# Optimization experiments

Measured on AMD Instinct MI355X. Metric: run time of the kernel, lower is better.

## Reference

```python
import jax, jax.numpy as jnp
import numpy as np

SIGNAL_LENGTH = 2048
BASE_STEP_SIZE = 0.01
MAX_ITERATIONS = 15
STEP_DECAY = 0.9
MIN_STEP = 1e-4
POS_TOL = 1e-4
EPS_SCALES = (0.001, 0.003, 0.01)
EPS_WEIGHTS = (0.5, 0.3, 0.2)


def setup_inputs() -> dict:
    key = jax.random.key(0)
    k1, k2 = jax.random.split(key)
    batch = 32768
    initial_predictions = jax.random.uniform(k1, (batch, 3), dtype=jnp.float32)
    signals = jax.random.normal(k2, (batch, SIGNAL_LENGTH), dtype=jnp.float32)
    return {"initial_predictions": initial_predictions, "signals": signals}


def _sample(signals, positions):
    # signals: [B, L], positions in [0,1]: [B, P] -> values [B, P]
    L = SIGNAL_LENGTH
    p = jnp.clip(positions * (L - 1), 0.0, float(L - 1))
    il = jnp.clip(jnp.floor(p).astype(jnp.int32), 0, L - 1)
    ir = jnp.clip(jnp.ceil(p).astype(jnp.int32), 0, L - 1)
    vl = jnp.take_along_axis(signals, il, axis=1)
    vr = jnp.take_along_axis(signals, ir, axis=1)
    wr = p - il.astype(p.dtype)
    return (1.0 - wr) * vl + wr * vr


def _grads_and_curvs(signals, positions):
    g_acc = 0.0
    c_acc = 0.0
    for eps, w in zip(EPS_SCALES, EPS_WEIGHTS):
        pc = jnp.clip(positions, eps, 1.0 - eps)
        v = _sample(signals, pc)
        vl = _sample(signals, pc - eps)
        vr = _sample(signals, pc + eps)
        g_acc = g_acc + w * (vr - vl) / (2.0 * eps)
        c_acc = c_acc + w * (vr + vl - 2.0 * v) / (eps * eps)
    return g_acc, jnp.clip(c_acc, -1000.0, 1000.0)


def _refine(initial_predictions, signals):
    positions = initial_predictions
    prev_positions = positions
    best_positions = positions
    best_values = _sample(signals, positions)
    step_size0 = jnp.asarray(BASE_STEP_SIZE, dtype=positions.dtype)
    done0 = jnp.asarray(False)

    def body(carry, it):
        positions, prev, best_pos, best_val, step_size, done = carry
        g, c = _grads_and_curvs(signals, positions)
        step = -g / (jnp.abs(c) + 1e-6)
        max_step = 0.2 * (STEP_DECAY ** it)
        step = jnp.clip(step, -max_step, max_step)
        new_pos = jnp.clip(positions + step_size * step, 0.0, 1.0)
        cur_val = _sample(signals, new_pos)
        # NOTE: original code sets best_positions = positions.clone() then
        # where(mask, positions, best_positions) -> best_positions == new_pos always
        new_best_pos = new_pos
        new_best_val = jnp.where(cur_val > best_val, cur_val, best_val)
        pos_change = jnp.max(jnp.abs(new_pos - prev))
        stop = (pos_change < POS_TOL) | (step_size < MIN_STEP)
        new_step = jnp.where(stop, step_size, step_size * STEP_DECAY)
        new_prev = jnp.where(stop, prev, new_pos)
        sel = lambda n, o: jnp.where(done, o, n)
        carry = (sel(new_pos, positions), sel(new_prev, prev),
                 sel(new_best_pos, best_pos), sel(new_best_val, best_val),
                 jnp.where(done, step_size, new_step), done | stop)
        return carry, None

    its = jnp.arange(MAX_ITERATIONS, dtype=positions.dtype)
    carry0 = (positions, prev_positions, best_positions, best_values, step_size0, done0)
    (_, _, best_positions, _, _, _), _ = jax.lax.scan(body, carry0, its)
    return best_positions


def reference(initial_predictions, signals):
    if signals.ndim == 3:
        signals = signals[:, 0, :]
    return _refine(initial_predictions, signals)
```

## Files before the change

kernel.cpp:

```cpp
#include <hip/hip_runtime.h>

#define SIG_LEN 2048
#define LM1F 2047.0f
#define N_ITER 15
#define TPB 128
#define WIN 96
#define WPAD 97

__device__ __forceinline__ float sample_lds(const float* __restrict__ w, float q) {
    float p = __fmul_rn(q, LM1F);
    p = fminf(fmaxf(p, 0.0f), LM1F);
    float fl = floorf(p);
    int il = (int)fl;
    int inc = (p > fl) ? 1 : 0;
    float wr = __fsub_rn(p, fl);
    float vl = w[il];
    float vr = w[il + inc];
    return __fadd_rn(__fmul_rn(__fsub_rn(1.0f, wr), vl), __fmul_rn(wr, vr));
}

__device__ __forceinline__ void fd_contrib(const float* __restrict__ w, float pos,
                                           float eps, float one_m_eps, float wgt,
                                           float two_eps, float eps_sq,
                                           float& g, float& c) {
    float pc = fminf(fmaxf(pos, eps), one_m_eps);
    float v  = sample_lds(w, pc);
    float vl = sample_lds(w, __fsub_rn(pc, eps));
    float vr = sample_lds(w, __fadd_rn(pc, eps));
    g = __fadd_rn(g, __fmul_rn(wgt, __fsub_rn(vr, vl)) / two_eps);
    float t = __fsub_rn(__fadd_rn(vr, vl), __fmul_rn(2.0f, v));
    c = __fadd_rn(c, __fmul_rn(wgt, t) / eps_sq);
}

__global__ __launch_bounds__(TPB) void refine_kernel(
    const float* __restrict__ init,
    const float* __restrict__ signals,
    float* __restrict__ out)
{
    __shared__ float win[TPB * WPAD];
    __shared__ int   wbase[TPB];

    const int tid   = threadIdx.x;
    const int task0 = blockIdx.x * TPB;
    const int task  = task0 + tid;

    const float p0 = init[task];
    float pp = fminf(fmaxf(__fmul_rn(p0, LM1F), 0.0f), LM1F);
    int base = (int)floorf(pp) - 47;
    base = min(max(base, 0), SIG_LEN - WIN);
    wbase[tid] = base;
    __syncthreads();

    #pragma unroll 4
    for (int k = tid; k < TPB * WIN; k += TPB) {
        int t = k / WIN;
        int e = k - t * WIN;
        int row = (task0 + t) / 3;
        win[t * WPAD + e] = signals[(size_t)row * SIG_LEN + (wbase[t] + e)];
    }
    __syncthreads();

    const float* __restrict__ w = &win[tid * WPAD] - base;

    float pos = p0;
    float ss = 0.01f;

    const float ms_tab[N_ITER] = {
        0.2f, 0.18f, 0.162f, 0.1458f, 0.13122f,
        0.118098f, 0.1062882f, 0.09565938f, 0.086093442f, 0.0774840978f,
        0.06973568802f, 0.062762119218f, 0.0564859072962f, 0.05083731656658f,
        0.045753584909922f
    };

    #pragma unroll
    for (int it = 0; it < N_ITER; ++it) {
        float g = 0.0f, c = 0.0f;
        fd_contrib(w, pos, 0.001f, 0.999f, 0.5f, 0.002f, 1e-06f, g, c);
        fd_contrib(w, pos, 0.003f, 0.997f, 0.3f, 0.006f, 9e-06f, g, c);
        fd_contrib(w, pos, 0.01f,  0.99f,  0.2f, 0.02f,  1e-04f, g, c);

        c = fminf(fmaxf(c, -1000.0f), 1000.0f);
        float step = (-g) / __fadd_rn(fabsf(c), 1e-06f);
        float ms = ms_tab[it];
        step = fminf(fmaxf(step, -ms), ms);
        pos = fminf(fmaxf(__fadd_rn(pos, __fmul_rn(ss, step)), 0.0f), 1.0f);
        ss = __fmul_rn(ss, 0.9f);
    }

    out[task] = pos;
}

extern "C" void kernel_launch(void* const* d_in, const int* in_sizes, int n_in,
                              void* d_out, int out_size, void* d_ws, size_t ws_size,
                              hipStream_t stream) {
    const float* init    = (const float*)d_in[0];
    const float* signals = (const float*)d_in[1];
    float* out = (float*)d_out;

    int n = out_size;
    int grid = n / TPB;
    refine_kernel<<<grid, TPB, 0, stream>>>(init, signals, out);
}
```

Measured before the change: 319.7 us.

## Vectorize window loads with float4 and batch LDS sample reads per iteration

The window base is aligned to a multiple of four so each thread's signal window can be fetched with float4 global loads instead of scalar loads. Inside each refinement iteration, all nine sample addresses are computed first, then the eighteen LDS reads are issued together before the interpolation math runs. This is meant to cut global load instruction count and to expose more memory-level parallelism on LDS reads, at the cost of extra register pressure. Aligning the base down by up to three elements shifts the window left, so positions near the right edge of the 96-element window could in principle fall outside it.

```diff
diff --git a/kernel.cpp b/kernel.cpp
--- a/kernel.cpp
+++ b/kernel.cpp
@@ -5,32 +5,9 @@
 #define N_ITER 15
 #define TPB 128
 #define WIN 96
+#define NF4 24
 #define WPAD 97
 
-__device__ __forceinline__ float sample_lds(const float* __restrict__ w, float q) {
-    float p = __fmul_rn(q, LM1F);
-    p = fminf(fmaxf(p, 0.0f), LM1F);
-    float fl = floorf(p);
-    int il = (int)fl;
-    int inc = (p > fl) ? 1 : 0;
-    float wr = __fsub_rn(p, fl);
-    float vl = w[il];
-    float vr = w[il + inc];
-    return __fadd_rn(__fmul_rn(__fsub_rn(1.0f, wr), vl), __fmul_rn(wr, vr));
-}
-
-__device__ __forceinline__ void fd_contrib(const float* __restrict__ w, float pos,
-                                           float eps, float one_m_eps, float wgt,
-                                           float two_eps, float eps_sq,
-                                           float& g, float& c) {
-    float pc = fminf(fmaxf(pos, eps), one_m_eps);
-    float v  = sample_lds(w, pc);
-    float vl = sample_lds(w, __fsub_rn(pc, eps));
-    float vr = sample_lds(w, __fadd_rn(pc, eps));
-    g = __fadd_rn(g, __fmul_rn(wgt, __fsub_rn(vr, vl)) / two_eps);
-    float t = __fsub_rn(__fadd_rn(vr, vl), __fmul_rn(2.0f, v));
-    c = __fadd_rn(c, __fmul_rn(wgt, t) / eps_sq);
-}
 
 __global__ __launch_bounds__(TPB) void refine_kernel(
     const float* __restrict__ init,
@@ -48,15 +25,22 @@
     float pp = fminf(fmaxf(__fmul_rn(p0, LM1F), 0.0f), LM1F);
     int base = (int)floorf(pp) - 47;
     base = min(max(base, 0), SIG_LEN - WIN);
+    base &= ~3;
     wbase[tid] = base;
     __syncthreads();
 
-    #pragma unroll 4
-    for (int k = tid; k < TPB * WIN; k += TPB) {
-        int t = k / WIN;
-        int e = k - t * WIN;
+    #pragma unroll
+    for (int k = tid; k < TPB * NF4; k += TPB) {
+        int t = k / NF4;
+        int j = k - t * NF4;
         int row = (task0 + t) / 3;
-        win[t * WPAD + e] = signals[(size_t)row * SIG_LEN + (wbase[t] + e)];
+        const float4 v = *reinterpret_cast<const float4*>(
+            &signals[(size_t)row * SIG_LEN + (wbase[t] + 4 * j)]);
+        int d = t * WPAD + 4 * j;
+        win[d]     = v.x;
+        win[d + 1] = v.y;
+        win[d + 2] = v.z;
+        win[d + 3] = v.w;
     }
     __syncthreads();
 
@@ -72,12 +56,56 @@
         0.045753584909922f
     };
 
+    const float eps_arr[3] = {0.001f, 0.003f, 0.01f};
+    const float ome_arr[3] = {0.999f, 0.997f, 0.99f};
+    const float wgt_arr[3] = {0.5f, 0.3f, 0.2f};
+    const float te_arr[3]  = {0.002f, 0.006f, 0.02f};
+    const float es_arr[3]  = {1e-06f, 9e-06f, 1e-04f};
+
     #pragma unroll
     for (int it = 0; it < N_ITER; ++it) {
+        int   adl[9], adr[9];
+        float wr9[9];
+        #pragma unroll
+        for (int s = 0; s < 3; ++s) {
+            float pc = fminf(fmaxf(pos, eps_arr[s]), ome_arr[s]);
+            float qs0 = pc;
+            float qs1 = __fsub_rn(pc, eps_arr[s]);
+            float qs2 = __fadd_rn(pc, eps_arr[s]);
+            float qs[3] = {qs0, qs1, qs2};
+            #pragma unroll
+            for (int u = 0; u < 3; ++u) {
+                const int i9 = s * 3 + u;
+                float p  = fminf(fmaxf(__fmul_rn(qs[u], LM1F), 0.0f), LM1F);
+                float fl = floorf(p);
+                int   il = (int)fl;
+                adl[i9] = il;
+                adr[i9] = il + ((p > fl) ? 1 : 0);
+                wr9[i9] = __fsub_rn(p, fl);
+            }
+        }
+        float vla[9], vra[9];
+        #pragma unroll
+        for (int i9 = 0; i9 < 9; ++i9) {
+            vla[i9] = w[adl[i9]];
+            vra[i9] = w[adr[i9]];
+        }
+        float sv[9];
+        #pragma unroll
+        for (int i9 = 0; i9 < 9; ++i9) {
+            sv[i9] = __fadd_rn(__fmul_rn(__fsub_rn(1.0f, wr9[i9]), vla[i9]),
+                               __fmul_rn(wr9[i9], vra[i9]));
+        }
         float g = 0.0f, c = 0.0f;
-        fd_contrib(w, pos, 0.001f, 0.999f, 0.5f, 0.002f, 1e-06f, g, c);
-        fd_contrib(w, pos, 0.003f, 0.997f, 0.3f, 0.006f, 9e-06f, g, c);
-        fd_contrib(w, pos, 0.01f,  0.99f,  0.2f, 0.02f,  1e-04f, g, c);
+        #pragma unroll
+        for (int s = 0; s < 3; ++s) {
+            float v  = sv[s * 3 + 0];
+            float vl = sv[s * 3 + 1];
+            float vr = sv[s * 3 + 2];
+            g = __fadd_rn(g, __fmul_rn(wgt_arr[s], __fsub_rn(vr, vl)) / te_arr[s]);
+            float t2 = __fsub_rn(__fadd_rn(vr, vl), __fmul_rn(2.0f, v));
+            c = __fadd_rn(c, __fmul_rn(wgt_arr[s], t2) / es_arr[s]);
+        }
 
         c = fminf(fmaxf(c, -1000.0f), 1000.0f);
         float step = (-g) / __fadd_rn(fabsf(c), 1e-06f);
```

After: 321.6 us. About the same (+0.6%).
